# Kernel optimization log

Measured on AMD Instinct MI355X. Metric: run time of the kernel, lower is better.

Reference implementation:

```python
import math
import jax, jax.numpy as jnp
import numpy as np

B, S, DIM = 1, 2048, 2880
N_HEADS, N_KV, HD = 64, 8, 64
ROPE_FACTOR = 32.0
THETA = 150000.0
NEG_INF = -1e30


def setup_inputs() -> dict:
    key = jax.random.key(0)
    ks = jax.random.split(key, 12)
    std = 0.02
    x = jax.random.normal(ks[0], (B, S, DIM), jnp.float32)
    # rope cache: (S, 2*HD) = [cos | sin], rotate_half convention (angles duplicated)
    inv_freq = 1.0 / (THETA ** (np.arange(0, HD, 2, dtype=np.float32) / HD))
    angles = np.arange(S, dtype=np.float32)[:, None] * inv_freq[None, :]   # (S, HD/2)
    emb = np.concatenate([angles, angles], axis=-1)                        # (S, HD)
    rope_cache = jnp.asarray(np.concatenate([np.cos(emb), np.sin(emb)], axis=-1))  # (S, 2*HD)
    wq_w = jax.random.normal(ks[1], (N_HEADS * HD, DIM), jnp.float32) * std
    wq_b = jax.random.normal(ks[2], (N_HEADS * HD,), jnp.float32) * std
    wk_w = jax.random.normal(ks[3], (N_KV * HD, DIM), jnp.float32) * std
    wk_b = jax.random.normal(ks[4], (N_KV * HD,), jnp.float32) * std
    wv_w = jax.random.normal(ks[5], (N_KV * HD, DIM), jnp.float32) * std
    wv_b = jax.random.normal(ks[6], (N_KV * HD,), jnp.float32) * std
    wo_w = jax.random.normal(ks[7], (DIM, N_HEADS * HD), jnp.float32) * std
    wo_b = jax.random.normal(ks[8], (DIM,), jnp.float32) * std
    sinks = jax.random.normal(ks[9], (N_HEADS,), jnp.float32) * std
    return {"x": x, "rope_cache": rope_cache, "wq_w": wq_w, "wq_b": wq_b,
            "wk_w": wk_w, "wk_b": wk_b, "wv_w": wv_w, "wv_b": wv_b,
            "wo_w": wo_w, "wo_b": wo_b, "sinks": sinks, "sliding_window": 128}


def _rotate_half(t):
    t1, t2 = t[..., : HD // 2], t[..., HD // 2 :]
    return jnp.concatenate([-t2, t1], axis=-1)


def reference(x, rope_cache, wq_w, wq_b, wk_w, wk_b, wv_w, wv_b, wo_w, wo_b, sinks, sliding_window):
    bsz, seqlen, _ = x.shape
    mscale = 0.1 * math.log(ROPE_FACTOR) + 1.0
    scale = mscale / math.sqrt(HD)

    q = (x @ wq_w.T + wq_b).reshape(bsz, seqlen, N_HEADS, HD)
    k = (x @ wk_w.T + wk_b).reshape(bsz, seqlen, N_KV, HD)
    v = (x @ wv_w.T + wv_b).reshape(bsz, seqlen, N_KV, HD)

    cos = rope_cache[:seqlen, :HD][None, :, None, :]   # (1,S,1,HD)
    sin = rope_cache[:seqlen, HD:][None, :, None, :]
    q = q * cos + _rotate_half(q) * sin
    k = k * cos + _rotate_half(k) * sin

    q = q.transpose(0, 2, 1, 3)                        # (B,H,S,hd)
    n_rep = N_HEADS // N_KV
    k = jnp.repeat(k.transpose(0, 2, 1, 3), n_rep, axis=1)  # GQA expand
    v = jnp.repeat(v.transpose(0, 2, 1, 3), n_rep, axis=1)

    scores = jnp.einsum("bhqd,bhkd->bhqk", q, k) * scale
    i = jnp.arange(seqlen)[:, None]
    j = jnp.arange(seqlen)[None, :]
    mask = (j <= i) & ((i - j) < sliding_window)       # causal + sliding window
    scores = jnp.where(mask[None, None], scores, NEG_INF)

    lse = jax.nn.logsumexp(scores, axis=-1)            # (B,H,S)
    attn = jax.nn.softmax(scores, axis=-1)
    out = jnp.einsum("bhqk,bhkd->bhqd", attn, v)

    sink_scale = jax.nn.sigmoid(lse - sinks[None, :, None])[..., None]
    out = out * sink_scale

    out = out.transpose(0, 2, 1, 3).reshape(bsz, seqlen, N_HEADS * HD)
    return out @ wo_w.T + wo_b
```

## Files before the change

### kernel.cpp

```cpp
#include <hip/hip_runtime.h>
#include <hip/hip_bf16.h>
#include <math.h>


typedef __bf16 bf16x8 __attribute__((ext_vector_type(8)));
typedef float  f32x4  __attribute__((ext_vector_type(4)));

#define MFMA_BF16(a,b,c) __builtin_amdgcn_mfma_f32_16x16x32_bf16((a),(b),(c),0,0,0)

#define XB   0L
#define WQB  5898240L
#define WKB  17694720L
#define WVB  19169280L
#define WOB  20643840L
#define QB   32440320L
#define KB   40828928L
#define VB   41877504L

__device__ __forceinline__ void gld_lds16(const void* g, void* l) {
    __builtin_amdgcn_global_load_lds(
        (__attribute__((address_space(1))) void*)(g),
        (__attribute__((address_space(3))) void*)(l), 16, 0, 0);
}

__device__ __forceinline__ bf16x8 ld8f(const float* p) {
    f32x4 a = *(const f32x4*)p;
    f32x4 b = *(const f32x4*)(p + 4);
    bf16x8 r;
#pragma unroll
    for (int t = 0; t < 4; t++) { r[t] = (__bf16)a[t]; r[t + 4] = (__bf16)b[t]; }
    return r;
}

__global__ __launch_bounds__(256) void convert_kernel(
    const float* __restrict__ x,  const float* __restrict__ wq,
    const float* __restrict__ wk, const float* __restrict__ wv,
    const float* __restrict__ wo, __bf16* __restrict__ dst)
{
    long e = ((long)blockIdx.x * 256 + threadIdx.x) * 8;
    const float* src; long off;
    if      (e <  WQB) { src = x;  off = e; }
    else if (e <  WKB) { src = wq; off = e - WQB; }
    else if (e <  WVB) { src = wk; off = e - WKB; }
    else if (e <  WOB) { src = wv; off = e - WVB; }
    else               { src = wo; off = e - WOB; }
    *(bf16x8*)(dst + e) = ld8f(src + off);
}

__device__ __forceinline__ void gemm_block64(
    const __bf16* __restrict__ A, const __bf16* __restrict__ W,
    const float* __restrict__ bias, __bf16* __restrict__ C,
    int N, int Ks, int kBeg, int kEnd, int m0, int n0,
    __bf16* As, __bf16* Bs)
{
    const int tid  = threadIdx.x;
    const int lane = tid & 63;
    const int wv   = tid >> 6;
    const int wm   = (wv >> 1) * 64;
    const int wn   = (wv & 1) * 64;
    const int quad = lane >> 4;
    const int c    = lane & 15;

    const int srow = tid >> 2;
    const int scol = (tid & 3) * 8;

    int br0 = n0 + srow;      if (br0 > N - 1) br0 = N - 1;
    int br1 = n0 + 64 + srow; if (br1 > N - 1) br1 = N - 1;
    const __bf16* pa0 = A + (size_t)(m0 + srow) * Ks + scol;
    const __bf16* pa1 = A + (size_t)(m0 + 64 + srow) * Ks + scol;
    const __bf16* pb0 = W + (size_t)br0 * Ks + scol;
    const __bf16* pb1 = W + (size_t)br1 * Ks + scol;

    f32x4 acc[4][4];
#pragma unroll
    for (int i = 0; i < 4; i++)
#pragma unroll
        for (int j = 0; j < 4; j++) acc[i][j] = (f32x4){0.f, 0.f, 0.f, 0.f};

    for (int kk = kBeg; kk < kEnd; kk += 64) {
        gld_lds16(pa0 + kk,      As + tid * 8);
        gld_lds16(pa1 + kk,      As + 2048 + tid * 8);
        gld_lds16(pa0 + kk + 32, As + 4096 + tid * 8);
        gld_lds16(pa1 + kk + 32, As + 6144 + tid * 8);
        gld_lds16(pb0 + kk,      Bs + tid * 8);
        gld_lds16(pb1 + kk,      Bs + 2048 + tid * 8);
        gld_lds16(pb0 + kk + 32, Bs + 4096 + tid * 8);
        gld_lds16(pb1 + kk + 32, Bs + 6144 + tid * 8);
        __syncthreads();
        for (int kt = 0; kt < 2; kt++) {
            bf16x8 af[4], bfv[4];
#pragma unroll
            for (int i = 0; i < 4; i++)
                af[i] = *(const bf16x8*)&As[kt * 4096 + (wm + i * 16 + c) * 32 + quad * 8];
#pragma unroll
            for (int j = 0; j < 4; j++)
                bfv[j] = *(const bf16x8*)&Bs[kt * 4096 + (wn + j * 16 + c) * 32 + quad * 8];
#pragma unroll
            for (int i = 0; i < 4; i++)
#pragma unroll
                for (int j = 0; j < 4; j++)
                    acc[i][j] = MFMA_BF16(af[i], bfv[j], acc[i][j]);
        }
        __syncthreads();
    }

#pragma unroll
    for (int j = 0; j < 4; j++) {
        int col = n0 + wn + j * 16 + c;
        if (col >= N) continue;
        float bv = bias ? bias[col] : 0.0f;
#pragma unroll
        for (int i = 0; i < 4; i++) {
            int row = m0 + wm + i * 16 + quad * 4;
#pragma unroll
            for (int r = 0; r < 4; r++)
                C[(size_t)(row + r) * N + col] = (__bf16)(acc[i][j][r] + bv);
        }
    }
}

__global__ __launch_bounds__(256, 3) void qkv_kernel(
    const __bf16* __restrict__ x,
    const __bf16* __restrict__ wq, const float* __restrict__ bq,
    const __bf16* __restrict__ wk, const float* __restrict__ bk,
    const __bf16* __restrict__ wv, const float* __restrict__ bv,
    __bf16* __restrict__ qo, __bf16* __restrict__ ko, __bf16* __restrict__ vo)
{
    __shared__ __align__(16) __bf16 As[8192], Bs[8192];
    const int by = blockIdx.y;
    const __bf16 *W; const float* bias; __bf16* C; int N, n0;
    if (by < 32)      { W = wq; bias = bq; C = qo; N = 4096; n0 = by * 128; }
    else if (by < 36) { W = wk; bias = bk; C = ko; N = 512;  n0 = (by - 32) * 128; }
    else              { W = wv; bias = bv; C = vo; N = 512;  n0 = (by - 36) * 128; }
    gemm_block64(x, W, bias, C, N, 2880, 0, 2880, blockIdx.x * 128, n0, As, Bs);
}

__global__ __launch_bounds__(256, 3) void oproj_kernel(
    const __bf16* __restrict__ a, const __bf16* __restrict__ w,
    __bf16* __restrict__ p0, __bf16* __restrict__ p1)
{
    __shared__ __align__(16) __bf16 As[8192], Bs[8192];
    const int z = blockIdx.z;
    __bf16* C = z ? p1 : p0;
    gemm_block64(a, w, nullptr, C, 2880, 4096, z * 2048, (z + 1) * 2048,
                 blockIdx.x * 128, blockIdx.y * 128, As, Bs);
}

__global__ __launch_bounds__(256) void reduce_kernel(
    const __bf16* __restrict__ p0, const __bf16* __restrict__ p1,
    const float* __restrict__ bo, float* __restrict__ out)
{
    long e = ((long)blockIdx.x * 256 + threadIdx.x) * 8;
    int col = (int)(e % 2880L);
    bf16x8 a = *(const bf16x8*)(p0 + e);
    bf16x8 b = *(const bf16x8*)(p1 + e);
    f32x4 o0, o1;
#pragma unroll
    for (int t = 0; t < 4; t++) {
        o0[t] = (float)a[t]     + (float)b[t]     + bo[col + t];
        o1[t] = (float)a[4 + t] + (float)b[4 + t] + bo[col + 4 + t];
    }
    *(f32x4*)(out + e)     = o0;
    *(f32x4*)(out + e + 4) = o1;
}

__global__ __launch_bounds__(256) void attn_kernel(
    __bf16* __restrict__ q, const __bf16* __restrict__ k,
    const __bf16* __restrict__ v, const float* __restrict__ sinks,
    const float* __restrict__ rope)
{
    __shared__ __align__(16) char smem[63488];
    __bf16* Qs = (__bf16*)smem;
    __bf16* Ks = (__bf16*)(smem + 9216);
    __bf16* Vt = (__bf16*)(smem + 36864);
    __bf16* P  = (__bf16*)smem;

    const int tid = threadIdx.x, lane = tid & 63, w = tid >> 6;
    const int quad = lane >> 4, c = lane & 15;
    const int i0 = blockIdx.x * 64;
    const int h  = blockIdx.y;
    const int kvh = h >> 3;
    const int k0 = i0 - 128;

    {
        const int srow = tid >> 2;
        const int dg   = (tid & 3) * 8;
        {
            const __bf16* gp = q + (size_t)(i0 + srow) * 4096 + h * 64 + dg;
            bf16x8 x1 = *(const bf16x8*)(gp);
            bf16x8 x2 = *(const bf16x8*)(gp + 32);
            const float* rc = rope + (size_t)(i0 + srow) * 128 + dg;
            bf16x8 o1, o2;
#pragma unroll
            for (int t = 0; t < 8; t++) {
                float cc = rc[t], si = rc[64 + t];
                float a = (float)x1[t], b = (float)x2[t];
                o1[t] = (__bf16)(a * cc - b * si);
                o2[t] = (__bf16)(b * cc + a * si);
            }
            *(bf16x8*)&Qs[srow * 72 + dg]      = o1;
            *(bf16x8*)&Qs[srow * 72 + dg + 32] = o2;
        }
#pragma unroll
        for (int it = 0; it < 3; it++) {
            int unit = it * 256 + tid;
            int krow = unit >> 2;
            int kdg  = (unit & 3) * 8;
            int j = k0 + krow; if (j < 0) j = 0;
            const __bf16* gp = k + (size_t)j * 512 + kvh * 64 + kdg;
            bf16x8 x1 = *(const bf16x8*)(gp);
            bf16x8 x2 = *(const bf16x8*)(gp + 32);
            const float* rc = rope + (size_t)j * 128 + kdg;
            bf16x8 o1, o2;
#pragma unroll
            for (int t = 0; t < 8; t++) {
                float cc = rc[t], si = rc[64 + t];
                float a = (float)x1[t], b = (float)x2[t];
                o1[t] = (__bf16)(a * cc - b * si);
                o2[t] = (__bf16)(b * cc + a * si);
            }
            *(bf16x8*)&Ks[krow * 72 + kdg]      = o1;
            *(bf16x8*)&Ks[krow * 72 + kdg + 32] = o2;
        }
        const int vrow = tid & 31;
        const int d0 = (tid >> 5) * 8;
#pragma unroll
        for (int it = 0; it < 6; it++) {
            int r2 = vrow + it * 32;
            int j = k0 + r2; if (j < 0) j = 0;
            bf16x8 t = *(const bf16x8*)(v + (size_t)j * 512 + kvh * 64 + d0);
#pragma unroll
            for (int u = 0; u < 8; u++) Vt[(d0 + u) * 208 + r2] = t[u];
        }
    }
    __syncthreads();

    f32x4 acc[12];
#pragma unroll
    for (int j = 0; j < 12; j++) acc[j] = (f32x4){0.f, 0.f, 0.f, 0.f};
#pragma unroll
    for (int kt = 0; kt < 2; kt++) {
        bf16x8 af = *(const bf16x8*)&Qs[(w * 16 + c) * 72 + kt * 32 + quad * 8];
#pragma unroll
        for (int j = 0; j < 12; j++) {
            bf16x8 bv = *(const bf16x8*)&Ks[(j * 16 + c) * 72 + kt * 32 + quad * 8];
            acc[j] = MFMA_BF16(af, bv, acc[j]);
        }
    }
    __syncthreads();

    const float scale = 0.16832169878499658f;
    const int igb = i0 + w * 16 + quad * 4;
    float rmax[4] = {-3.0e4f, -3.0e4f, -3.0e4f, -3.0e4f};
#pragma unroll
    for (int j = 0; j < 12; j++) {
        int jg = k0 + j * 16 + c;
#pragma unroll
        for (int r = 0; r < 4; r++) {
            int ig = igb + r;
            bool ok = (jg >= 0) && (jg <= ig) && (ig - jg < 128);
            float vv = ok ? acc[j][r] * scale : -3.0e4f;
            acc[j][r] = vv;
            rmax[r] = fmaxf(rmax[r], vv);
        }
    }
#pragma unroll
    for (int off = 1; off < 16; off <<= 1)
#pragma unroll
        for (int r = 0; r < 4; r++)
            rmax[r] = fmaxf(rmax[r], __shfl_xor(rmax[r], off));

    float rs[4] = {0.f, 0.f, 0.f, 0.f};
#pragma unroll
    for (int j = 0; j < 12; j++)
#pragma unroll
        for (int r = 0; r < 4; r++) {
            float e = __expf(acc[j][r] - rmax[r]);
            acc[j][r] = e;
            rs[r] += e;
        }
#pragma unroll
    for (int off = 1; off < 16; off <<= 1)
#pragma unroll
        for (int r = 0; r < 4; r++)
            rs[r] += __shfl_xor(rs[r], off);

    float rowfac[4];
    {
        float sk = sinks[h];
#pragma unroll
        for (int r = 0; r < 4; r++) {
            float s = fmaxf(rs[r], 1e-20f);
            float lse = rmax[r] + __logf(s);
            rowfac[r] = 1.f / ((1.f + __expf(sk - lse)) * s);
        }
    }

#pragma unroll
    for (int j = 0; j < 12; j++)
#pragma unroll
        for (int r = 0; r < 4; r++)
            P[(w * 16 + quad * 4 + r) * 208 + j * 16 + c] = (__bf16)acc[j][r];
    __syncthreads();

    f32x4 acc2[4];
#pragma unroll
    for (int jd = 0; jd < 4; jd++) acc2[jd] = (f32x4){0.f, 0.f, 0.f, 0.f};
#pragma unroll
    for (int kt = 0; kt < 6; kt++) {
        bf16x8 a = *(const bf16x8*)&P[(w * 16 + c) * 208 + kt * 32 + quad * 8];
#pragma unroll
        for (int jd = 0; jd < 4; jd++) {
            bf16x8 b = *(const bf16x8*)&Vt[(jd * 16 + c) * 208 + kt * 32 + quad * 8];
            acc2[jd] = MFMA_BF16(a, b, acc2[jd]);
        }
    }
#pragma unroll
    for (int jd = 0; jd < 4; jd++)
#pragma unroll
        for (int r = 0; r < 4; r++) {
            int qr = w * 16 + quad * 4 + r;
            q[(size_t)(i0 + qr) * 4096 + h * 64 + jd * 16 + c] =
                (__bf16)(acc2[jd][r] * rowfac[r]);
        }
}

extern "C" void kernel_launch(void* const* d_in, const int* in_sizes, int n_in,
                              void* d_out, int out_size, void* d_ws, size_t ws_size,
                              hipStream_t stream) {
    const float* x    = (const float*)d_in[0];
    const float* rope = (const float*)d_in[1];
    const float* wq   = (const float*)d_in[2];
    const float* bq   = (const float*)d_in[3];
    const float* wk   = (const float*)d_in[4];
    const float* bk   = (const float*)d_in[5];
    const float* wv   = (const float*)d_in[6];
    const float* bv   = (const float*)d_in[7];
    const float* wo   = (const float*)d_in[8];
    const float* bo   = (const float*)d_in[9];
    const float* sk   = (const float*)d_in[10];
    float* out = (float*)d_out;

    __bf16* wsb = (__bf16*)d_ws;
    __bf16* xb  = wsb + XB;
    __bf16* wqb = wsb + WQB;
    __bf16* wkb = wsb + WKB;
    __bf16* wvb = wsb + WVB;
    __bf16* wob = wsb + WOB;
    __bf16* qb  = wsb + QB;
    __bf16* kb  = wsb + KB;
    __bf16* vb  = wsb + VB;
    __bf16* po0 = wsb + 0L;
    __bf16* po1 = wsb + 5898240L;

    convert_kernel<<<15840, 256, 0, stream>>>(x, wq, wk, wv, wo, xb);
    qkv_kernel<<<dim3(16, 40), 256, 0, stream>>>(xb, wqb, bq, wkb, bk, wvb, bv,
                                                 qb, kb, vb);
    attn_kernel<<<dim3(32, 64), 256, 0, stream>>>(qb, kb, vb, sk, rope);
    oproj_kernel<<<dim3(16, 23, 2), 256, 0, stream>>>(qb, wob, po0, po1);
    reduce_kernel<<<2880, 256, 0, stream>>>(po0, po1, bo, out);
}
```

Baseline: 340.0 us.

## Share K/V tiles across GQA heads and keep attention probabilities in registers

Each attention block now covers one KV head and all eight query heads that share it, one wave per head, with 512 threads. Rotated K and transposed V are loaded into LDS once per block instead of once per query head. The score matmul is computed transposed (K as the A operand), only the 9 key tiles inside the sliding-window band are computed, and P is rearranged with lane shuffles into the layout the PV matmul needs, so the LDS round-trip and two barriers go away. The attention scale is folded into the Q rope, and s_setprio hints are placed around the MFMA loops. In exchange the block count falls from 2048 to 256, the cross-lane shuffle and mask logic is more complex, and register pressure rises.

```diff
diff --git a/kernel.cpp b/kernel.cpp
--- a/kernel.cpp
+++ b/kernel.cpp
@@ -1,10 +1,12 @@
 #include <hip/hip_runtime.h>
 #include <hip/hip_bf16.h>
 #include <math.h>
+#include <stdint.h>
 
 
 typedef __bf16 bf16x8 __attribute__((ext_vector_type(8)));
 typedef float  f32x4  __attribute__((ext_vector_type(4)));
+typedef uint32_t u32x4 __attribute__((ext_vector_type(4)));
 
 #define MFMA_BF16(a,b,c) __builtin_amdgcn_mfma_f32_16x16x32_bf16((a),(b),(c),0,0,0)
 
@@ -30,6 +32,12 @@
 #pragma unroll
     for (int t = 0; t < 4; t++) { r[t] = (__bf16)a[t]; r[t + 4] = (__bf16)b[t]; }
     return r;
+}
+
+__device__ __forceinline__ uint32_t pack2(float a, float b) {
+    __bf16 x = (__bf16)a, y = (__bf16)b;
+    return (uint32_t)__builtin_bit_cast(unsigned short, x)
+         | ((uint32_t)__builtin_bit_cast(unsigned short, y) << 16);
 }
 
 __global__ __launch_bounds__(256) void convert_kernel(
@@ -164,46 +172,26 @@
     *(f32x4*)(out + e + 4) = o1;
 }
 
-__global__ __launch_bounds__(256) void attn_kernel(
+__global__ __launch_bounds__(512) void attn_kernel(
     __bf16* __restrict__ q, const __bf16* __restrict__ k,
     const __bf16* __restrict__ v, const float* __restrict__ sinks,
     const float* __restrict__ rope)
 {
-    __shared__ __align__(16) char smem[63488];
-    __bf16* Qs = (__bf16*)smem;
-    __bf16* Ks = (__bf16*)(smem + 9216);
-    __bf16* Vt = (__bf16*)(smem + 36864);
-    __bf16* P  = (__bf16*)smem;
+    __shared__ __align__(16) __bf16 Ks[192 * 72];
+    __shared__ __align__(16) __bf16 Vt[64 * 200];
 
     const int tid = threadIdx.x, lane = tid & 63, w = tid >> 6;
     const int quad = lane >> 4, c = lane & 15;
-    const int i0 = blockIdx.x * 64;
-    const int h  = blockIdx.y;
-    const int kvh = h >> 3;
-    const int k0 = i0 - 128;
-
-    {
-        const int srow = tid >> 2;
-        const int dg   = (tid & 3) * 8;
-        {
-            const __bf16* gp = q + (size_t)(i0 + srow) * 4096 + h * 64 + dg;
-            bf16x8 x1 = *(const bf16x8*)(gp);
-            bf16x8 x2 = *(const bf16x8*)(gp + 32);
-            const float* rc = rope + (size_t)(i0 + srow) * 128 + dg;
-            bf16x8 o1, o2;
-#pragma unroll
-            for (int t = 0; t < 8; t++) {
-                float cc = rc[t], si = rc[64 + t];
-                float a = (float)x1[t], b = (float)x2[t];
-                o1[t] = (__bf16)(a * cc - b * si);
-                o2[t] = (__bf16)(b * cc + a * si);
-            }
-            *(bf16x8*)&Qs[srow * 72 + dg]      = o1;
-            *(bf16x8*)&Qs[srow * 72 + dg + 32] = o2;
-        }
-#pragma unroll
-        for (int it = 0; it < 3; it++) {
-            int unit = it * 256 + tid;
+    const int i0  = blockIdx.x * 64;
+    const int kvh = blockIdx.y;
+    const int h   = kvh * 8 + w;
+    const int k0  = i0 - 128;
+    const float scale = 0.16832169878499658f;
+
+#pragma unroll
+    for (int it = 0; it < 2; it++) {
+        int unit = it * 512 + tid;
+        if (unit < 768) {
             int krow = unit >> 2;
             int kdg  = (unit & 3) * 8;
             int j = k0 + krow; if (j < 0) j = 0;
@@ -222,107 +210,141 @@
             *(bf16x8*)&Ks[krow * 72 + kdg]      = o1;
             *(bf16x8*)&Ks[krow * 72 + kdg + 32] = o2;
         }
-        const int vrow = tid & 31;
-        const int d0 = (tid >> 5) * 8;
-#pragma unroll
-        for (int it = 0; it < 6; it++) {
-            int r2 = vrow + it * 32;
-            int j = k0 + r2; if (j < 0) j = 0;
+    }
+
+    {
+        const int vrow = tid & 63;
+        const int d0   = (tid >> 6) * 8;
+#pragma unroll
+        for (int it = 0; it < 3; it++) {
+            int s = it * 64 + vrow;
+            int j = k0 + s; if (j < 0) j = 0;
             bf16x8 t = *(const bf16x8*)(v + (size_t)j * 512 + kvh * 64 + d0);
 #pragma unroll
-            for (int u = 0; u < 8; u++) Vt[(d0 + u) * 208 + r2] = t[u];
-        }
-    }
+            for (int u = 0; u < 8; u++) Vt[(d0 + u) * 200 + s] = t[u];
+        }
+    }
+
+    bf16x8 qf[4][2];
+#pragma unroll
+    for (int f = 0; f < 4; f++) {
+        const int row = i0 + f * 16 + c;
+        const __bf16* gp = q + (size_t)row * 4096 + h * 64 + quad * 8;
+        bf16x8 x1 = *(const bf16x8*)(gp);
+        bf16x8 x2 = *(const bf16x8*)(gp + 32);
+        const float* rc = rope + (size_t)row * 128 + quad * 8;
+        bf16x8 o1, o2;
+#pragma unroll
+        for (int t = 0; t < 8; t++) {
+            float cc = rc[t] * scale, si = rc[64 + t] * scale;
+            float a = (float)x1[t], b = (float)x2[t];
+            o1[t] = (__bf16)(a * cc - b * si);
+            o2[t] = (__bf16)(b * cc + a * si);
+        }
+        qf[f][0] = o1; qf[f][1] = o2;
+    }
+
     __syncthreads();
 
-    f32x4 acc[12];
-#pragma unroll
-    for (int j = 0; j < 12; j++) acc[j] = (f32x4){0.f, 0.f, 0.f, 0.f};
-#pragma unroll
-    for (int kt = 0; kt < 2; kt++) {
-        bf16x8 af = *(const bf16x8*)&Qs[(w * 16 + c) * 72 + kt * 32 + quad * 8];
-#pragma unroll
-        for (int j = 0; j < 12; j++) {
-            bf16x8 bv = *(const bf16x8*)&Ks[(j * 16 + c) * 72 + kt * 32 + quad * 8];
-            acc[j] = MFMA_BF16(af, bv, acc[j]);
-        }
-    }
-    __syncthreads();
-
-    const float scale = 0.16832169878499658f;
-    const int igb = i0 + w * 16 + quad * 4;
-    float rmax[4] = {-3.0e4f, -3.0e4f, -3.0e4f, -3.0e4f};
-#pragma unroll
-    for (int j = 0; j < 12; j++) {
-        int jg = k0 + j * 16 + c;
-#pragma unroll
-        for (int r = 0; r < 4; r++) {
-            int ig = igb + r;
-            bool ok = (jg >= 0) && (jg <= ig) && (ig - jg < 128);
-            float vv = ok ? acc[j][r] * scale : -3.0e4f;
-            acc[j][r] = vv;
-            rmax[r] = fmaxf(rmax[r], vv);
-        }
-    }
-#pragma unroll
-    for (int off = 1; off < 16; off <<= 1)
-#pragma unroll
-        for (int r = 0; r < 4; r++)
-            rmax[r] = fmaxf(rmax[r], __shfl_xor(rmax[r], off));
-
-    float rs[4] = {0.f, 0.f, 0.f, 0.f};
-#pragma unroll
-    for (int j = 0; j < 12; j++)
-#pragma unroll
-        for (int r = 0; r < 4; r++) {
-            float e = __expf(acc[j][r] - rmax[r]);
-            acc[j][r] = e;
-            rs[r] += e;
-        }
-#pragma unroll
-    for (int off = 1; off < 16; off <<= 1)
-#pragma unroll
-        for (int r = 0; r < 4; r++)
-            rs[r] += __shfl_xor(rs[r], off);
-
-    float rowfac[4];
-    {
-        float sk = sinks[h];
-#pragma unroll
-        for (int r = 0; r < 4; r++) {
-            float s = fmaxf(rs[r], 1e-20f);
-            float lse = rmax[r] + __logf(s);
-            rowfac[r] = 1.f / ((1.f + __expf(sk - lse)) * s);
-        }
-    }
-
-#pragma unroll
-    for (int j = 0; j < 12; j++)
-#pragma unroll
-        for (int r = 0; r < 4; r++)
-            P[(w * 16 + quad * 4 + r) * 208 + j * 16 + c] = (__bf16)acc[j][r];
-    __syncthreads();
-
-    f32x4 acc2[4];
-#pragma unroll
-    for (int jd = 0; jd < 4; jd++) acc2[jd] = (f32x4){0.f, 0.f, 0.f, 0.f};
-#pragma unroll
-    for (int kt = 0; kt < 6; kt++) {
-        bf16x8 a = *(const bf16x8*)&P[(w * 16 + c) * 208 + kt * 32 + quad * 8];
-#pragma unroll
-        for (int jd = 0; jd < 4; jd++) {
-            bf16x8 b = *(const bf16x8*)&Vt[(jd * 16 + c) * 208 + kt * 32 + quad * 8];
-            acc2[jd] = MFMA_BF16(a, b, acc2[jd]);
-        }
-    }
-#pragma unroll
-    for (int jd = 0; jd < 4; jd++)
-#pragma unroll
-        for (int r = 0; r < 4; r++) {
-            int qr = w * 16 + quad * 4 + r;
-            q[(size_t)(i0 + qr) * 4096 + h * 64 + jd * 16 + c] =
-                (__bf16)(acc2[jd][r] * rowfac[r]);
-        }
+    const float sk   = sinks[h];
+    const int laneA  = ((quad & 1) << 5) + c;
+    const int laneB  = laneA + 16;
+    const bool hiSel = (quad >> 1) != 0;
+    const int db     = 128 + c - quad * 4;
+
+#pragma unroll
+    for (int f = 0; f < 4; f++) {
+        f32x4 acc9[9];
+#pragma unroll
+        for (int jj = 0; jj < 9; jj++) acc9[jj] = (f32x4){0.f, 0.f, 0.f, 0.f};
+        __builtin_amdgcn_s_setprio(1);
+#pragma unroll
+        for (int jj = 0; jj < 9; jj++) {
+            const int j = f + jj;
+#pragma unroll
+            for (int kt = 0; kt < 2; kt++) {
+                bf16x8 kf = *(const bf16x8*)&Ks[(j * 16 + c) * 72 + kt * 32 + quad * 8];
+                acc9[jj] = MFMA_BF16(kf, qf[f][kt], acc9[jj]);
+            }
+        }
+        __builtin_amdgcn_s_setprio(0);
+
+        const int jgb = k0 + f * 16 + quad * 4;
+        float rmax = -3.0e4f;
+#pragma unroll
+        for (int jj = 0; jj < 9; jj++)
+#pragma unroll
+            for (int r = 0; r < 4; r++) {
+                int d  = db  - jj * 16 - r;
+                int jg = jgb + jj * 16 + r;
+                bool ok = ((unsigned)d < 128u) && (jg >= 0);
+                float vv = ok ? acc9[jj][r] : -3.0e4f;
+                acc9[jj][r] = vv;
+                rmax = fmaxf(rmax, vv);
+            }
+        rmax = fmaxf(rmax, __shfl_xor(rmax, 16));
+        rmax = fmaxf(rmax, __shfl_xor(rmax, 32));
+
+        float rs = 0.f;
+#pragma unroll
+        for (int jj = 0; jj < 9; jj++)
+#pragma unroll
+            for (int r = 0; r < 4; r++) {
+                float e = __expf(acc9[jj][r] - rmax);
+                acc9[jj][r] = e;
+                rs += e;
+            }
+        rs += __shfl_xor(rs, 16);
+        rs += __shfl_xor(rs, 32);
+
+        float s   = fmaxf(rs, 1e-20f);
+        float lse = rmax + __logf(s);
+        float fac = 1.f / ((1.f + __expf(sk - lse)) * s);
+
+        uint32_t pk[24];
+#pragma unroll
+        for (int t = 0; t < 24; t++) pk[t] = 0;
+#pragma unroll
+        for (int jj = 0; jj < 9; jj++) {
+            const int j = f + jj;
+            pk[2 * j]     = pack2(acc9[jj][0] * fac, acc9[jj][1] * fac);
+            pk[2 * j + 1] = pack2(acc9[jj][2] * fac, acc9[jj][3] * fac);
+        }
+
+        f32x4 acc2[4];
+#pragma unroll
+        for (int jd = 0; jd < 4; jd++) acc2[jd] = (f32x4){0.f, 0.f, 0.f, 0.f};
+        const int kt0 = f >> 1;
+#pragma unroll
+        for (int kk = 0; kk < 5; kk++) {
+            const int kt = kt0 + kk;
+            uint32_t l0  = (uint32_t)__shfl((int)pk[4 * kt],     laneA);
+            uint32_t h0  = (uint32_t)__shfl((int)pk[4 * kt + 1], laneA);
+            uint32_t l0b = (uint32_t)__shfl((int)pk[4 * kt],     laneB);
+            uint32_t h0b = (uint32_t)__shfl((int)pk[4 * kt + 1], laneB);
+            uint32_t l1  = (uint32_t)__shfl((int)pk[4 * kt + 2], laneA);
+            uint32_t h1  = (uint32_t)__shfl((int)pk[4 * kt + 3], laneA);
+            uint32_t l1b = (uint32_t)__shfl((int)pk[4 * kt + 2], laneB);
+            uint32_t h1b = (uint32_t)__shfl((int)pk[4 * kt + 3], laneB);
+            u32x4 wv = { hiSel ? l1  : l0,  hiSel ? h1  : h0,
+                         hiSel ? l1b : l0b, hiSel ? h1b : h0b };
+            bf16x8 pa = __builtin_bit_cast(bf16x8, wv);
+            __builtin_amdgcn_s_setprio(1);
+#pragma unroll
+            for (int jd = 0; jd < 4; jd++) {
+                bf16x8 bv = *(const bf16x8*)&Vt[(jd * 16 + c) * 200 + kt * 32 + quad * 8];
+                acc2[jd] = MFMA_BF16(pa, bv, acc2[jd]);
+            }
+            __builtin_amdgcn_s_setprio(0);
+        }
+
+#pragma unroll
+        for (int jd = 0; jd < 4; jd++)
+#pragma unroll
+            for (int r = 0; r < 4; r++)
+                q[(size_t)(i0 + f * 16 + quad * 4 + r) * 4096 + h * 64 + jd * 16 + c]
+                    = (__bf16)acc2[jd][r];
+    }
 }
 
 extern "C" void kernel_launch(void* const* d_in, const int* in_sizes, int n_in,
@@ -356,7 +378,7 @@
     convert_kernel<<<15840, 256, 0, stream>>>(x, wq, wk, wv, wo, xb);
     qkv_kernel<<<dim3(16, 40), 256, 0, stream>>>(xb, wqb, bq, wkb, bk, wvb, bv,
                                                  qb, kb, vb);
-    attn_kernel<<<dim3(32, 64), 256, 0, stream>>>(qb, kb, vb, sk, rope);
+    attn_kernel<<<dim3(32, 8), 512, 0, stream>>>(qb, kb, vb, sk, rope);
     oproj_kernel<<<dim3(16, 23, 2), 256, 0, stream>>>(qb, wob, po0, po1);
     reduce_kernel<<<2880, 256, 0, stream>>>(po0, po1, bo, out);
 }
```

New measurement: 332.6 us. -2.2%, faster.
